# Performance work log

Hardware: AMD Instinct MI355X
Metric: run time of the kernel (lower is better)

## Reference

```python
import jax, jax.numpy as jnp
import numpy as np
from jax import lax

# Model dims (match init_kwargs / input_specs)
B, S, D = 4, 2048, 1024
L, H, K = 4, 4, 4
DH = D // H            # 256 head dim
UP = 1344              # ceil(1.3*D/64)*64, gated FFN proj dim
EPS = 1e-5


def _ln(x, w):
    # xlstm LayerNorm: weight only, no bias
    mu = x.mean(-1, keepdims=True)
    var = x.var(-1, keepdims=True)
    return (x - mu) * lax.rsqrt(var + EPS) * w


def _slstm_layer(xn, cw, cb, wi, wf, wz, wo, rk, b, gnw):
    # xn: (B,S,D). Causal depthwise conv1d + swish feeds i/f gates; z/o from xn.
    Bc, Sc, Dc = xn.shape
    xc = lax.conv_general_dilated(
        xn.transpose(0, 2, 1), cw[:, None, :], (1,), [(K - 1, 0)],
        dimension_numbers=("NCH", "OIH", "NCH"), feature_group_count=Dc)
    xc = jax.nn.silu(xc + cb[None, :, None]).transpose(0, 2, 1)
    hx = xc.reshape(Bc, Sc, H, DH)
    hz = xn.reshape(Bc, Sc, H, DH)
    # LinearHeadwiseExpand: block-diagonal per-head linear, no bias
    gi = jnp.einsum("bshd,hod->bsho", hx, wi)
    gf = jnp.einsum("bshd,hod->bsho", hx, wf)
    gz = jnp.einsum("bshd,hod->bsho", hz, wz)
    go = jnp.einsum("bshd,hod->bsho", hz, wo)
    wx = jnp.stack([gi, gf, gz, go], axis=3)  # (B,S,H,4,DH)

    def step(carry, wx_t):
        h, c, n, m = carry  # each (B,H,DH)
        raw = wx_t + jnp.einsum("bhd,hdgo->bhgo", h, rk) + b  # (B,H,4,DH)
        ir, fr, zr, og = raw[:, :, 0], raw[:, :, 1], raw[:, :, 2], raw[:, :, 3]
        lfm = m + jax.nn.log_sigmoid(fr)
        mn = jnp.maximum(ir, lfm)          # stabilizer state
        ig = jnp.exp(ir - mn)
        fg = jnp.exp(lfm - mn)
        cn = fg * c + ig * jnp.tanh(zr)
        nn = fg * n + ig
        hn = jax.nn.sigmoid(og) * cn / nn
        return (hn, cn, nn, mn), hn

    z0 = jnp.zeros((Bc, H, DH), xn.dtype)
    _, ys = lax.scan(step, (z0, z0, z0, z0), jnp.moveaxis(wx, 1, 0))
    y = jnp.moveaxis(ys, 0, 1)  # (B,S,H,DH)
    # MultiHeadLayerNorm / GroupNorm(num_groups=H), weight only
    mu = y.mean(-1, keepdims=True)
    var = y.var(-1, keepdims=True)
    y = (y - mu) * lax.rsqrt(var + EPS) * gnw.reshape(H, DH)
    return y.reshape(Bc, Sc, Dc)


def _ffn(xn, wu, wd):
    u = xn @ wu
    g, v = u[..., :UP], u[..., UP:]
    return (jax.nn.gelu(g, approximate=False) * v) @ wd


def setup_inputs() -> dict:
    key = jax.random.key(0)
    ks = jax.random.split(key, 9)
    sg = DH ** -0.5
    return {
        "x": jax.random.normal(ks[0], (B, S, D), jnp.float32),
        "ln1_w": jnp.ones((L, D), jnp.float32),
        "conv_w": jax.random.normal(ks[1], (L, D, K), jnp.float32) * 0.1,
        "conv_b": jnp.zeros((L, D), jnp.float32),
        "wi": jax.random.normal(ks[2], (L, H, DH, DH), jnp.float32) * sg,
        "wf": jax.random.normal(ks[3], (L, H, DH, DH), jnp.float32) * sg,
        "wz": jax.random.normal(ks[4], (L, H, DH, DH), jnp.float32) * sg,
        "wo": jax.random.normal(ks[5], (L, H, DH, DH), jnp.float32) * sg,
        "rker": jax.random.normal(ks[6], (L, H, DH, 4, DH), jnp.float32) * sg,
        "cell_b": jax.random.normal(ks[7], (L, H, 4, DH), jnp.float32) * 0.1,
        "gn_w": jnp.ones((L, D), jnp.float32),
        "ln2_w": jnp.ones((L, D), jnp.float32),
        "ff_up": jax.random.normal(ks[8], (L, D, 2 * UP), jnp.float32) * (D ** -0.5),
        "ff_down": jax.random.normal(jax.random.fold_in(key, 99), (L, UP, D), jnp.float32) * (UP ** -0.5),
        "post_w": jnp.ones((D,), jnp.float32),
    }


def reference(x, ln1_w, conv_w, conv_b, wi, wf, wz, wo, rker, cell_b, gn_w, ln2_w, ff_up, ff_down, post_w):
    for l in range(L):
        x = x + _slstm_layer(_ln(x, ln1_w[l]), conv_w[l], conv_b[l],
                             wi[l], wf[l], wz[l], wo[l], rker[l], cell_b[l], gn_w[l])
        x = x + _ffn(_ln(x, ln2_w[l]), ff_up[l], ff_down[l])
    return _ln(x, post_w)  # post-blocks norm; dropout is identity in eval
```

## Files before the change

### kernel.cpp

```cpp
#include <hip/hip_runtime.h>
#include <hip/hip_bf16.h>
#include <hip/hip_fp16.h>
#include <math.h>


typedef unsigned int  u32;
typedef unsigned short u16;
typedef __hip_bfloat16 bf16;

typedef short bf16x8 __attribute__((ext_vector_type(8)));
typedef float f32x4  __attribute__((ext_vector_type(4)));
typedef _Float16 half2t __attribute__((ext_vector_type(2)));

#define EPSF 1e-5f
#define SIGF32 0x3F800000u

__device__ __forceinline__ float bfu2f(u16 u){ return __uint_as_float(((u32)u) << 16); }
__device__ __forceinline__ float ldm(const void* p, long i, int f32){
  return f32 ? ((const float*)p)[i] : bfu2f(((const u16*)p)[i]);
}
__device__ __forceinline__ float qdot(u32 w, u32 hp, float acc){
#if defined(__has_builtin)
#if __has_builtin(__builtin_amdgcn_fdot2)
  return __builtin_amdgcn_fdot2(__builtin_bit_cast(half2t, w),
                                __builtin_bit_cast(half2t, hp), acc, false);
#else
  half2t a = __builtin_bit_cast(half2t, w);
  half2t b = __builtin_bit_cast(half2t, hp);
  acc = fmaf((float)a.x, (float)b.x, acc);
  return fmaf((float)a.y, (float)b.y, acc);
#endif
#else
  half2t a = __builtin_bit_cast(half2t, w);
  half2t b = __builtin_bit_cast(half2t, hp);
  acc = fmaf((float)a.x, (float)b.x, acc);
  return fmaf((float)a.y, (float)b.y, acc);
#endif
}

__global__ __launch_bounds__(256) void k_canary(const u32* __restrict__ sig,
                                                void* __restrict__ out, int n, float code){
  int f32 = (sig[0] == SIGF32);
  int i = blockIdx.x*256 + threadIdx.x;
  if (i >= n) return;
  float v = (i == 0) ? code : 0.f;
  if (f32) ((float*)out)[i] = v;
  else     ((bf16*)out)[i]  = __float2bfloat16(v);
}

__global__ __launch_bounds__(256) void k_cast(const void* __restrict__ in,
                                              const u32* __restrict__ sig,
                                              float* __restrict__ out){
  int f32 = (sig[0] == SIGF32);
  long i = (long)blockIdx.x*256 + threadIdx.x;
  if (f32){
    ((float4*)out)[i] = ((const float4*)in)[i];
  } else {
    ushort4 v = ((const ushort4*)in)[i];
    float4 f;
    f.x = bfu2f(v.x); f.y = bfu2f(v.y); f.z = bfu2f(v.z); f.w = bfu2f(v.w);
    ((float4*)out)[i] = f;
  }
}

__global__ __launch_bounds__(256) void k_cvt(const void* __restrict__ src, long off,
                                             const u32* __restrict__ sig,
                                             bf16* __restrict__ dst, int n){
  int f32 = (sig[0] == SIGF32);
  int i = blockIdx.x*256 + threadIdx.x;
  if (i < n) dst[i] = __float2bfloat16(ldm(src, off + i, f32));
}

__global__ __launch_bounds__(256) void k_ln(const float* __restrict__ X,
                                            const void* __restrict__ w, long woff,
                                            const u32* __restrict__ sig,
                                            void* __restrict__ out, int outf){
  int f32 = (sig[0] == SIGF32);
  int row = blockIdx.x, t = threadIdx.x;
  float4 xv = ((const float4*)(X + (long)row*1024))[t];
  float s1 = xv.x + xv.y + xv.z + xv.w;
  float s2 = xv.x*xv.x + xv.y*xv.y + xv.z*xv.z + xv.w*xv.w;
  #pragma unroll
  for (int off = 32; off >= 1; off >>= 1){ s1 += __shfl_xor(s1, off); s2 += __shfl_xor(s2, off); }
  __shared__ float rb[8];
  if ((t & 63) == 0){ rb[t>>6] = s1; rb[4 + (t>>6)] = s2; }
  __syncthreads();
  s1 = rb[0]+rb[1]+rb[2]+rb[3];
  s2 = rb[4]+rb[5]+rb[6]+rb[7];
  float mu  = s1 * (1.f/1024.f);
  float var = s2 * (1.f/1024.f) - mu*mu;
  float rs  = rsqrtf(fmaxf(var, 0.f) + EPSF);
  float xs[4] = {xv.x, xv.y, xv.z, xv.w};
  #pragma unroll
  for (int j = 0; j < 4; j++){
    float val = (xs[j]-mu)*rs*ldm(w, woff + t*4 + j, f32);
    long oi = (long)row*1024 + t*4 + j;
    if (outf && f32) ((float*)out)[oi] = val;
    else             ((bf16*)out)[oi]  = __float2bfloat16(val);
  }
}

__global__ __launch_bounds__(256) void k_conv(const bf16* __restrict__ XN,
                                              const void* __restrict__ cw, long cwoff,
                                              const void* __restrict__ cb, long cboff,
                                              const u32* __restrict__ sig,
                                              bf16* __restrict__ WX){
  int f32 = (sig[0] == SIGF32);
  int idx = blockIdx.x*256 + threadIdx.x;
  int c = idx & 1023;
  int s = (idx >> 10) & 2047;
  int b = idx >> 21;
  float acc = ldm(cb, cboff + c, f32);
  const bf16* xp = XN + idx;
  #pragma unroll
  for (int k = 0; k < 4; k++){
    int sk = s - 3 + k;
    float xv = (sk >= 0) ? (float)xp[(k-3)*1024] : 0.f;
    acc += xv * ldm(cw, cwoff + c*4 + k, f32);
  }
  float sg = 1.f / (1.f + __expf(-acc));
  WX[(long)b*8388608 + (long)(c>>8)*2097152 + (long)s*1024 + 512 + (c & 255)]
      = __float2bfloat16(acc * sg);
}

__global__ __launch_bounds__(256) void k_packrk(const void* __restrict__ rk, long off,
                                                const u32* __restrict__ sig,
                                                u32* __restrict__ rkReg,
                                                u32* __restrict__ rkLds,
                                                u32* __restrict__ rkStr){
  int f32 = (sig[0] == SIGF32);
  int idx = blockIdx.x*256 + threadIdx.x;
  if (idx >= 524288) return;
  int dp = idx & 127;
  int gc = (idx >> 7) & 1023;
  int h  = idx >> 17;
  long p = off + (long)h*262144 + (long)(dp*2)*1024 + gc;
  float a = ldm(rk, p, f32);
  float b = ldm(rk, p + 1024, f32);
  u32 lo = (u32)__builtin_bit_cast(u16, (_Float16)a);
  u32 hi = (u32)__builtin_bit_cast(u16, (_Float16)b);
  u32 v = lo | (hi << 16);
  if (dp < 64){
    rkReg[((long)dp*4 + h)*1024 + gc] = v;
  } else if (dp < 88){
    int k = (dp-64)>>2, j = (dp-64)&3;
    rkLds[((long)(h*6 + k)*1024 + gc)*4 + j] = v;
  } else {
    int pg = (dp-88)>>2, j = (dp-88)&3;
    rkStr[((long)(h*10 + pg)*1024 + gc)*4 + j] = v;
  }
}

__global__ __launch_bounds__(256) void k_transpose(const void* __restrict__ in, long off,
                                                   const u32* __restrict__ sig,
                                                   bf16* __restrict__ out, int R, int C){
  int f32 = (sig[0] == SIGF32);
  __shared__ bf16 tile[32][33];
  int tx = threadIdx.x & 31, ty = threadIdx.x >> 5;
  int r0 = blockIdx.y*32, c0 = blockIdx.x*32;
  #pragma unroll
  for (int i = 0; i < 4; i++)
    tile[ty + i*8][tx] = __float2bfloat16(ldm(in, off + (long)(r0 + ty + i*8)*C + c0 + tx, f32));
  __syncthreads();
  #pragma unroll
  for (int i = 0; i < 4; i++) out[(long)(c0 + ty + i*8)*R + r0 + tx] = tile[tx][ty + i*8];
}

__global__ __launch_bounds__(256) void k_gemm(const bf16* __restrict__ A, int lda, int aoff, int agate,
                                              const bf16* __restrict__ B0,
                                              const bf16* __restrict__ B1, int ldb, int nsplit,
                                              int K, int mode,
                                              bf16* __restrict__ outb, int ldo, int woff,
                                              float* __restrict__ resid){
  int lane = threadIdx.x & 63, wv = threadIdx.x >> 6;
  int wrow = wv >> 1, wcol = wv & 1;
  int m15 = lane & 15, q = lane >> 4;
  int mBase = blockIdx.x*128 + wrow*64;
  int nBase = blockIdx.y*128 + wcol*64;

  const bf16* Ap[4]; const bf16* Bp[4];
  #pragma unroll
  for (int i = 0; i < 4; i++){
    int row = mBase + i*16 + m15;
    long abase = agate ? ((long)(row >> 11)*8388608 + (long)(row & 2047)*1024)
                       : ((long)row*lda);
    Ap[i] = A + abase + aoff + q*8;
    int n = nBase + i*16 + m15;
    const bf16* bb = (n < nsplit) ? (B0 + (long)n*ldb) : (B1 + (long)(n - nsplit)*ldb);
    Bp[i] = bb + q*8;
  }
  f32x4 acc[4][4];
  f32x4 zero = {0.f, 0.f, 0.f, 0.f};
  #pragma unroll
  for (int i = 0; i < 4; i++)
    #pragma unroll
    for (int j = 0; j < 4; j++) acc[i][j] = zero;

  for (int k0 = 0; k0 < K; k0 += 32){
    bf16x8 af[4], bfg[4];
    #pragma unroll
    for (int i = 0; i < 4; i++){ af[i]  = *reinterpret_cast<const bf16x8*>(Ap[i]); Ap[i] += 32; }
    #pragma unroll
    for (int i = 0; i < 4; i++){ bfg[i] = *reinterpret_cast<const bf16x8*>(Bp[i]); Bp[i] += 32; }
    #pragma unroll
    for (int i = 0; i < 4; i++)
      #pragma unroll
      for (int j = 0; j < 4; j++)
        acc[i][j] = __builtin_amdgcn_mfma_f32_16x16x32_bf16(af[i], bfg[j], acc[i][j], 0, 0, 0);
  }

  #pragma unroll
  for (int i = 0; i < 4; i++){
    #pragma unroll
    for (int j = 0; j < 4; j++){
      #pragma unroll
      for (int r = 0; r < 4; r++){
        int row = mBase + i*16 + q*4 + r;
        int col = nBase + j*16 + m15;
        float v = acc[i][j][r];
        if (mode == 0){
          outb[(long)row*ldo + col] = __float2bfloat16(v);
        } else if (mode == 1){
          outb[(long)(row >> 11)*8388608 + (long)(row & 2047)*1024 + woff + col] = __float2bfloat16(v);
        } else {
          resid[(long)row*1024 + col] += v;
        }
      }
    }
  }
}

__global__ __launch_bounds__(256) void k_act(const bf16* __restrict__ U, bf16* __restrict__ E){
  int idx = blockIdx.x*256 + threadIdx.x;
  int row = idx / 1344;
  int j   = idx - row*1344;
  float g = (float)U[(long)row*2688 + j];
  float v = (float)U[(long)row*2688 + 1344 + j];
  float ge = 0.5f * g * (1.f + erff(g * 0.70710678118654752f));
  E[idx] = __float2bfloat16(ge * v);
}

__global__ __launch_bounds__(1024, 4) void k_recur(const bf16* __restrict__ WX,
                                                const u32*  __restrict__ rkReg,
                                                const uint4* __restrict__ rkLdsG,
                                                const uint4* __restrict__ rkStrG,
                                                const void* __restrict__ cb, long cboff,
                                                const void* __restrict__ gnw, long gnoff,
                                                const u32*  __restrict__ sig,
                                                float* __restrict__ X,
                                                int szero){
  int f32 = (sig[0] == SIGF32);
  int bh = blockIdx.x;
  int b = bh >> 2, h = bh & 3;
  int tid = threadIdx.x;
  int cell = tid & 255;

  u32 wreg[64];
  {
    const u32* rg = rkReg + h*1024 + tid;
    #pragma unroll
    for (int i = 0; i < 64; i++) wreg[i] = rg[i*4096];
  }
  #pragma unroll
  for (int i = 0; i < 64; i++) asm volatile("" : "+v"(wreg[i]));

  __shared__ __align__(16) uint4 wlds[6144];
  __shared__ __align__(16) float araw[1024];
  __shared__ __align__(16) u16 hs16[256];
  __shared__ float rbuf[8];
  {
    const uint4* srcL = rkLdsG + h*6144;
    #pragma unroll
    for (int k = 0; k < 6; k++) wlds[k*1024 + tid] = srcL[k*1024 + tid];
  }

  const uint4* st = rkStrG + h*10240 + tid;

  float bias = ldm(cb, cboff + h*1024 + tid, f32);
  float gw   = ldm(gnw, gnoff + h*256 + cell, f32);

  if (tid < 256) hs16[tid] = 0;
  __syncthreads();

  float c = 0.f, n = 0.f, m = 0.f;
  const u16* wxu = (const u16*)(WX + (long)bh*2097152) + tid;
  float* Xp = X + (long)b*2097152 + h*256 + cell;

  u16 wxc = wxu[0];
  for (int s = 0; s < 2048; s++){
    u16 wxn = wxu[(s < 2047) ? 1024 : 0];
    int off = s * szero;
    const uint4* hq = (const uint4*)hs16;

    float acc = bias + bfu2f(wxc);
    #pragma unroll
    for (int j2 = 0; j2 < 16; j2++){
      uint4 hv = hq[j2];
      acc = qdot(wreg[4*j2+0], hv.x, acc);
      acc = qdot(wreg[4*j2+1], hv.y, acc);
      acc = qdot(wreg[4*j2+2], hv.z, acc);
      acc = qdot(wreg[4*j2+3], hv.w, acc);
    }
    #pragma unroll
    for (int k = 0; k < 6; k++){
      uint4 q = wlds[k*1024 + tid + off];
      uint4 hv = hq[16+k];
      acc = qdot(q.x, hv.x, acc); acc = qdot(q.y, hv.y, acc);
      acc = qdot(q.z, hv.z, acc); acc = qdot(q.w, hv.w, acc);
    }
    #pragma unroll
    for (int pg = 0; pg < 10; pg++){
      uint4 q = st[pg*1024 + off];
      uint4 hv = hq[22+pg];
      acc = qdot(q.x, hv.x, acc); acc = qdot(q.y, hv.y, acc);
      acc = qdot(q.z, hv.z, acc); acc = qdot(q.w, hv.w, acc);
    }
    araw[tid] = acc;
    __syncthreads();

    float y = 0.f;
    if (tid < 256){
      float a0 = araw[cell], a1 = araw[256+cell], a2 = araw[512+cell], a3 = araw[768+cell];
      float e1   = __expf(-fabsf(a1));
      float lsig = fminf(a1, 0.f) - __logf(1.f + e1);
      float lfm  = m + lsig;
      float mn   = fmaxf(a0, lfm);
      float ig   = __expf(a0 - mn);
      float fg   = __expf(lfm - mn);
      float t2   = __expf(-2.f*fabsf(a2));
      float th   = __builtin_copysignf(__fdividef(1.f - t2, 1.f + t2), a2);
      float cn   = fg*c + ig*th;
      float nn   = fg*n + ig;
      float sg   = __fdividef(1.f, 1.f + __expf(-a3));
      float hn   = sg * __fdividef(cn, nn);
      c = cn; n = nn; m = mn;
      hs16[cell] = __builtin_bit_cast(u16, (_Float16)hn);
      float r1 = hn, r2 = hn*hn;
      #pragma unroll
      for (int o2 = 32; o2 >= 1; o2 >>= 1){ r1 += __shfl_xor(r1, o2); r2 += __shfl_xor(r2, o2); }
      if ((tid & 63) == 0){ rbuf[tid>>6] = r1; rbuf[4 + (tid>>6)] = r2; }
      y = hn;
    }
    __syncthreads();

    if (tid < 256){
      float S1 = rbuf[0]+rbuf[1]+rbuf[2]+rbuf[3];
      float S2 = rbuf[4]+rbuf[5]+rbuf[6]+rbuf[7];
      float mu  = S1 * (1.f/256.f);
      float var = S2 * (1.f/256.f) - mu*mu;
      *Xp += (y - mu) * rsqrtf(fmaxf(var, 0.f) + EPSF) * gw;
    }
    Xp += 1024;
    wxu += 1024;
    wxc = wxn;
  }
}

extern "C" void kernel_launch(void* const* d_in, const int* in_sizes, int n_in,
                              void* d_out, int out_size, void* d_ws, size_t ws_size,
                              hipStream_t stream){
  const void* x_in   = d_in[0];
  const void* ln1_w  = d_in[1];
  const void* conv_w = d_in[2];
  const void* conv_b = d_in[3];
  const void* wi     = d_in[4];
  const void* wf     = d_in[5];
  const void* wz     = d_in[6];
  const void* wo     = d_in[7];
  const void* rker   = d_in[8];
  const void* cell_b = d_in[9];
  const void* gn_w   = d_in[10];
  const void* ln2_w  = d_in[11];
  const void* ff_up  = d_in[12];
  const void* ff_dn  = d_in[13];
  const void* post_w = d_in[14];
  const u32* sig = (const u32*)ln1_w;

  if (ws_size < 134217728ULL){
    k_canary<<<(out_size+255)/256, 256, 0, stream>>>(sig, d_out, out_size, 4000.f);
    return;
  }
  if (n_in < 15 || in_sizes[0] != 8388608 || in_sizes[8] != 4194304 ||
      in_sizes[12] != 11010048 || out_size != 8388608){
    k_canary<<<(out_size+255)/256, 256, 0, stream>>>(sig, d_out, out_size, 8000.f);
    return;
  }

  char* ws = (char*)d_ws;
  float* X    = (float*)(ws + 0);
  bf16*  XN   = (bf16*) (ws + 33554432);
  u32*   rkReg= (u32*)  (ws + 50331648);
  u32*   rkLds= (u32*)  (ws + 50331648 + 1048576);
  u32*   rkStr= (u32*)  (ws + 50331648 + 1441792);
  bf16*  gW   = (bf16*) (ws + 50331648 + 2097152);
  bf16*  fupT = (bf16*) (ws + 50331648 + 4194304);
  bf16*  fdnT = (bf16*) (ws + 50331648 + 9699328);
  bf16*  WX   = (bf16*) (ws + 67108864);
  bf16*  U    = WX;
  bf16*  E    = (bf16*) (ws + 67108864 + 44040192);

  k_cast<<<8192, 256, 0, stream>>>(x_in, sig, X);

  for (int l = 0; l < 4; l++){
    k_ln<<<8192, 256, 0, stream>>>(X, ln1_w, (long)l*1024, sig, XN, 0);
    k_conv<<<32768, 256, 0, stream>>>(XN, conv_w, (long)l*4096, conv_b, (long)l*1024, sig, WX);

    k_cvt<<<1024, 256, 0, stream>>>(wi, (long)l*262144, sig, gW +      0, 262144);
    k_cvt<<<1024, 256, 0, stream>>>(wf, (long)l*262144, sig, gW + 262144, 262144);
    k_cvt<<<1024, 256, 0, stream>>>(wz, (long)l*262144, sig, gW + 524288, 262144);
    k_cvt<<<1024, 256, 0, stream>>>(wo, (long)l*262144, sig, gW + 786432, 262144);

    for (int h = 0; h < 4; h++){
      k_gemm<<<dim3(64,4), 256, 0, stream>>>(WX, 0, h*2097152 + 512, 1,
          gW + h*65536, gW + 262144 + h*65536, 256, 256,
          256, 1, WX, 0, h*2097152 + 0, nullptr);
    }
    k_packrk<<<2048, 256, 0, stream>>>(rker, (long)l*1048576, sig, rkReg, rkLds, rkStr);
    for (int h = 0; h < 4; h++){
      k_gemm<<<dim3(64,4), 256, 0, stream>>>(XN, 1024, h*256, 0,
          gW + 524288 + h*65536, gW + 786432 + h*65536, 256, 256,
          256, 1, WX, 0, h*2097152 + 512, nullptr);
    }

    k_recur<<<16, 1024, 0, stream>>>(WX, rkReg, (const uint4*)rkLds, (const uint4*)rkStr,
                                     cell_b, (long)l*4096, gn_w, (long)l*1024, sig, X, 0);

    k_ln<<<8192, 256, 0, stream>>>(X, ln2_w, (long)l*1024, sig, XN, 0);
    k_transpose<<<dim3(84,32), 256, 0, stream>>>(ff_up, (long)l*2752512, sig, fupT, 1024, 2688);
    k_gemm<<<dim3(64,21), 256, 0, stream>>>(XN, 1024, 0, 0, fupT, fupT, 1024, 1<<30,
        1024, 0, U, 2688, 0, nullptr);
    k_act<<<43008, 256, 0, stream>>>(U, E);
    k_transpose<<<dim3(32,42), 256, 0, stream>>>(ff_dn, (long)l*1376256, sig, fdnT, 1344, 1024);
    k_gemm<<<dim3(64,8), 256, 0, stream>>>(E, 1344, 0, 0, fdnT, fdnT, 1344, 1<<30,
        1344, 2, nullptr, 0, 0, X);
  }

  k_ln<<<8192, 256, 0, stream>>>(X, post_w, 0, sig, d_out, 1);
}
```

Measured before the change: 26.62 ms.

## Split recurrent matvec across four thread quarters and move GroupNorm to separate kernel

The recurrent kernel now assigns each thread a quarter of the hidden dimension for all four gates of a cell. Partial sums are reduced with cross-lane shuffles instead of being staged through shared memory. Register weights drop from 64 to 48 words per thread, and h is replicated into four padded shared copies to avoid bank conflicts. The per-step GroupNorm and residual add are taken out of the serial loop: hidden states are written as fp16 into the WX buffer and a new parallel k_gn kernel applies the norm afterwards. In exchange each step does more shuffles and strided global loads, and the norm adds an extra kernel with its own memory traffic.

```diff
diff --git a/kernel.cpp b/kernel.cpp
--- a/kernel.cpp
+++ b/kernel.cpp
@@ -19,6 +19,7 @@
 __device__ __forceinline__ float ldm(const void* p, long i, int f32){
   return f32 ? ((const float*)p)[i] : bfu2f(((const u16*)p)[i]);
 }
+__device__ __forceinline__ float f16u2f(u16 u){ return (float)__builtin_bit_cast(_Float16, u); }
 __device__ __forceinline__ float qdot(u32 w, u32 hp, float acc){
 #if defined(__has_builtin)
 #if __has_builtin(__builtin_amdgcn_fdot2)
@@ -134,20 +135,22 @@
   int dp = idx & 127;
   int gc = (idx >> 7) & 1023;
   int h  = idx >> 17;
+  int g  = gc >> 8, cell = gc & 255;
+  int q  = dp >> 5, i = dp & 31;
+  int tid = (cell >> 4)*64 + q*16 + (cell & 15);
   long p = off + (long)h*262144 + (long)(dp*2)*1024 + gc;
   float a = ldm(rk, p, f32);
   float b = ldm(rk, p + 1024, f32);
   u32 lo = (u32)__builtin_bit_cast(u16, (_Float16)a);
   u32 hi = (u32)__builtin_bit_cast(u16, (_Float16)b);
   u32 v = lo | (hi << 16);
-  if (dp < 64){
-    rkReg[((long)dp*4 + h)*1024 + gc] = v;
-  } else if (dp < 88){
-    int k = (dp-64)>>2, j = (dp-64)&3;
-    rkLds[((long)(h*6 + k)*1024 + gc)*4 + j] = v;
+  if (i < 12){
+    rkReg[((long)(g*12 + i)*4 + h)*1024 + tid] = v;
+  } else if (i < 16){
+    rkLds[(((long)(h*4 + g))*1024 + tid)*4 + (i - 12)] = v;
   } else {
-    int pg = (dp-88)>>2, j = (dp-88)&3;
-    rkStr[((long)(h*10 + pg)*1024 + gc)*4 + j] = v;
+    int c = (i-16) >> 2, j = (i-16) & 3;
+    rkStr[(((long)(h*16 + g*4 + c))*1024 + tid)*4 + j] = v;
   }
 }
 
@@ -240,87 +243,98 @@
   E[idx] = __float2bfloat16(ge * v);
 }
 
-__global__ __launch_bounds__(1024, 4) void k_recur(const bf16* __restrict__ WX,
+__global__ __launch_bounds__(1024, 4) void k_recur(bf16* __restrict__ WX,
                                                 const u32*  __restrict__ rkReg,
                                                 const uint4* __restrict__ rkLdsG,
                                                 const uint4* __restrict__ rkStrG,
                                                 const void* __restrict__ cb, long cboff,
-                                                const void* __restrict__ gnw, long gnoff,
                                                 const u32*  __restrict__ sig,
-                                                float* __restrict__ X,
                                                 int szero){
   int f32 = (sig[0] == SIGF32);
   int bh = blockIdx.x;
-  int b = bh >> 2, h = bh & 3;
+  int h = bh & 3;
   int tid = threadIdx.x;
-  int cell = tid & 255;
-
-  u32 wreg[64];
+  int celllo = tid & 15, q = (tid >> 4) & 3, cellhi = tid >> 6;
+  int cell = cellhi*16 + celllo;
+
+  u32 wreg[48];
   {
     const u32* rg = rkReg + h*1024 + tid;
     #pragma unroll
-    for (int i = 0; i < 64; i++) wreg[i] = rg[i*4096];
-  }
-  #pragma unroll
-  for (int i = 0; i < 64; i++) asm volatile("" : "+v"(wreg[i]));
-
-  __shared__ __align__(16) uint4 wlds[6144];
-  __shared__ __align__(16) float araw[1024];
-  __shared__ __align__(16) u16 hs16[256];
-  __shared__ float rbuf[8];
+    for (int i = 0; i < 48; i++) wreg[i] = rg[i*4096];
+  }
+  #pragma unroll
+  for (int i = 0; i < 48; i++) asm volatile("" : "+v"(wreg[i]));
+
+  __shared__ __align__(16) uint4 wlds[4096];
+  __shared__ __align__(16) u16 hsr[4*264];
   {
-    const uint4* srcL = rkLdsG + h*6144;
-    #pragma unroll
-    for (int k = 0; k < 6; k++) wlds[k*1024 + tid] = srcL[k*1024 + tid];
-  }
-
-  const uint4* st = rkStrG + h*10240 + tid;
-
-  float bias = ldm(cb, cboff + h*1024 + tid, f32);
-  float gw   = ldm(gnw, gnoff + h*256 + cell, f32);
-
-  if (tid < 256) hs16[tid] = 0;
+    const uint4* srcL = rkLdsG + h*4096;
+    #pragma unroll
+    for (int g = 0; g < 4; g++) wlds[g*1024 + tid] = srcL[g*1024 + tid];
+  }
+  if (tid < 528) ((u32*)hsr)[tid] = 0;
+
+  const uint4* st = rkStrG + h*16384 + tid;
+  float bias = ldm(cb, cboff + h*1024 + q*256 + cell, f32);
+
   __syncthreads();
 
   float c = 0.f, n = 0.f, m = 0.f;
-  const u16* wxu = (const u16*)(WX + (long)bh*2097152) + tid;
-  float* Xp = X + (long)b*2097152 + h*256 + cell;
+  const u16* wxu = (const u16*)WX + (long)bh*2097152 + q*256 + cell;
+  u16* yout = (u16*)WX + (long)bh*2097152 + cell;
 
   u16 wxc = wxu[0];
   for (int s = 0; s < 2048; s++){
     u16 wxn = wxu[(s < 2047) ? 1024 : 0];
     int off = s * szero;
-    const uint4* hq = (const uint4*)hs16;
-
-    float acc = bias + bfu2f(wxc);
-    #pragma unroll
-    for (int j2 = 0; j2 < 16; j2++){
-      uint4 hv = hq[j2];
-      acc = qdot(wreg[4*j2+0], hv.x, acc);
-      acc = qdot(wreg[4*j2+1], hv.y, acc);
-      acc = qdot(wreg[4*j2+2], hv.z, acc);
-      acc = qdot(wreg[4*j2+3], hv.w, acc);
+
+    const uint4* hq = ((const uint4*)hsr) + q*41;
+    uint4 hh0 = hq[0+off], hh1 = hq[1+off], hh2 = hq[2+off], hh3 = hq[3+off];
+    uint4 hh4 = hq[4+off], hh5 = hq[5+off], hh6 = hq[6+off], hh7 = hq[7+off];
+
+    float p0, p1, p2, p3;
+    #pragma unroll
+    for (int g = 0; g < 4; g++){
+      uint4 s0 = st[(g*4+0)*1024 + off];
+      uint4 s1 = st[(g*4+1)*1024 + off];
+      uint4 s2 = st[(g*4+2)*1024 + off];
+      uint4 s3 = st[(g*4+3)*1024 + off];
+      uint4 wl = wlds[g*1024 + tid + off];
+      const u32* wr = wreg + g*12;
+      float a = 0.f;
+      a = qdot(wr[0],  hh0.x, a); a = qdot(wr[1],  hh0.y, a);
+      a = qdot(wr[2],  hh0.z, a); a = qdot(wr[3],  hh0.w, a);
+      a = qdot(wr[4],  hh1.x, a); a = qdot(wr[5],  hh1.y, a);
+      a = qdot(wr[6],  hh1.z, a); a = qdot(wr[7],  hh1.w, a);
+      a = qdot(wr[8],  hh2.x, a); a = qdot(wr[9],  hh2.y, a);
+      a = qdot(wr[10], hh2.z, a); a = qdot(wr[11], hh2.w, a);
+      a = qdot(wl.x, hh3.x, a); a = qdot(wl.y, hh3.y, a);
+      a = qdot(wl.z, hh3.z, a); a = qdot(wl.w, hh3.w, a);
+      a = qdot(s0.x, hh4.x, a); a = qdot(s0.y, hh4.y, a);
+      a = qdot(s0.z, hh4.z, a); a = qdot(s0.w, hh4.w, a);
+      a = qdot(s1.x, hh5.x, a); a = qdot(s1.y, hh5.y, a);
+      a = qdot(s1.z, hh5.z, a); a = qdot(s1.w, hh5.w, a);
+      a = qdot(s2.x, hh6.x, a); a = qdot(s2.y, hh6.y, a);
+      a = qdot(s2.z, hh6.z, a); a = qdot(s2.w, hh6.w, a);
+      a = qdot(s3.x, hh7.x, a); a = qdot(s3.y, hh7.y, a);
+      a = qdot(s3.z, hh7.z, a); a = qdot(s3.w, hh7.w, a);
+      if (g == 0) p0 = a; else if (g == 1) p1 = a; else if (g == 2) p2 = a; else p3 = a;
     }
-    #pragma unroll
-    for (int k = 0; k < 6; k++){
-      uint4 q = wlds[k*1024 + tid + off];
-      uint4 hv = hq[16+k];
-      acc = qdot(q.x, hv.x, acc); acc = qdot(q.y, hv.y, acc);
-      acc = qdot(q.z, hv.z, acc); acc = qdot(q.w, hv.w, acc);
-    }
-    #pragma unroll
-    for (int pg = 0; pg < 10; pg++){
-      uint4 q = st[pg*1024 + off];
-      uint4 hv = hq[22+pg];
-      acc = qdot(q.x, hv.x, acc); acc = qdot(q.y, hv.y, acc);
-      acc = qdot(q.z, hv.z, acc); acc = qdot(q.w, hv.w, acc);
-    }
-    araw[tid] = acc;
+    float addv = bias + bfu2f(wxc);
+    p0 += (q == 0) ? addv : 0.f;
+    p1 += (q == 1) ? addv : 0.f;
+    p2 += (q == 2) ? addv : 0.f;
+    p3 += (q == 3) ? addv : 0.f;
+    p0 += __shfl_xor(p0, 16); p0 += __shfl_xor(p0, 32);
+    p1 += __shfl_xor(p1, 16); p1 += __shfl_xor(p1, 32);
+    p2 += __shfl_xor(p2, 16); p2 += __shfl_xor(p2, 32);
+    p3 += __shfl_xor(p3, 16); p3 += __shfl_xor(p3, 32);
+
     __syncthreads();
 
-    float y = 0.f;
-    if (tid < 256){
-      float a0 = araw[cell], a1 = araw[256+cell], a2 = araw[512+cell], a3 = araw[768+cell];
+    if (q == 0){
+      float a0 = p0, a1 = p1, a2 = p2, a3 = p3;
       float e1   = __expf(-fabsf(a1));
       float lsig = fminf(a1, 0.f) - __logf(1.f + e1);
       float lfm  = m + lsig;
@@ -334,26 +348,40 @@
       float sg   = __fdividef(1.f, 1.f + __expf(-a3));
       float hn   = sg * __fdividef(cn, nn);
       c = cn; n = nn; m = mn;
-      hs16[cell] = __builtin_bit_cast(u16, (_Float16)hn);
-      float r1 = hn, r2 = hn*hn;
-      #pragma unroll
-      for (int o2 = 32; o2 >= 1; o2 >>= 1){ r1 += __shfl_xor(r1, o2); r2 += __shfl_xor(r2, o2); }
-      if ((tid & 63) == 0){ rbuf[tid>>6] = r1; rbuf[4 + (tid>>6)] = r2; }
-      y = hn;
+      u16 h16 = __builtin_bit_cast(u16, (_Float16)hn);
+      hsr[0*264 + cell] = h16; hsr[1*264 + cell] = h16;
+      hsr[2*264 + cell] = h16; hsr[3*264 + cell] = h16;
+      yout[(long)s*1024] = h16;
     }
     __syncthreads();
 
-    if (tid < 256){
-      float S1 = rbuf[0]+rbuf[1]+rbuf[2]+rbuf[3];
-      float S2 = rbuf[4]+rbuf[5]+rbuf[6]+rbuf[7];
-      float mu  = S1 * (1.f/256.f);
-      float var = S2 * (1.f/256.f) - mu*mu;
-      *Xp += (y - mu) * rsqrtf(fmaxf(var, 0.f) + EPSF) * gw;
-    }
-    Xp += 1024;
     wxu += 1024;
     wxc = wxn;
   }
+}
+
+__global__ __launch_bounds__(256) void k_gn(const u16* __restrict__ Y,
+                                            const void* __restrict__ gnw, long gnoff,
+                                            const u32* __restrict__ sig,
+                                            float* __restrict__ X){
+  int f32 = (sig[0] == SIGF32);
+  int r = blockIdx.x;
+  int bh = r >> 11, s = r & 2047, b = bh >> 2, h = bh & 3;
+  int t = threadIdx.x;
+  float y = f16u2f(Y[(long)bh*2097152 + (long)s*1024 + t]);
+  float s1 = y, s2 = y*y;
+  #pragma unroll
+  for (int off = 32; off >= 1; off >>= 1){ s1 += __shfl_xor(s1, off); s2 += __shfl_xor(s2, off); }
+  __shared__ float rb[8];
+  if ((t & 63) == 0){ rb[t>>6] = s1; rb[4 + (t>>6)] = s2; }
+  __syncthreads();
+  s1 = rb[0]+rb[1]+rb[2]+rb[3];
+  s2 = rb[4]+rb[5]+rb[6]+rb[7];
+  float mu  = s1 * (1.f/256.f);
+  float var = s2 * (1.f/256.f) - mu*mu;
+  float rs  = rsqrtf(fmaxf(var, 0.f) + EPSF);
+  float gw  = ldm(gnw, gnoff + h*256 + t, f32);
+  X[(long)b*2097152 + (long)s*1024 + h*256 + t] += (y - mu)*rs*gw;
 }
 
 extern "C" void kernel_launch(void* const* d_in, const int* in_sizes, int n_in,
@@ -390,8 +418,8 @@
   float* X    = (float*)(ws + 0);
   bf16*  XN   = (bf16*) (ws + 33554432);
   u32*   rkReg= (u32*)  (ws + 50331648);
-  u32*   rkLds= (u32*)  (ws + 50331648 + 1048576);
-  u32*   rkStr= (u32*)  (ws + 50331648 + 1441792);
+  u32*   rkLds= (u32*)  (ws + 50331648 + 786432);
+  u32*   rkStr= (u32*)  (ws + 50331648 + 1048576);
   bf16*  gW   = (bf16*) (ws + 50331648 + 2097152);
   bf16*  fupT = (bf16*) (ws + 50331648 + 4194304);
   bf16*  fdnT = (bf16*) (ws + 50331648 + 9699328);
@@ -423,7 +451,8 @@
     }
 
     k_recur<<<16, 1024, 0, stream>>>(WX, rkReg, (const uint4*)rkLds, (const uint4*)rkStr,
-                                     cell_b, (long)l*4096, gn_w, (long)l*1024, sig, X, 0);
+                                     cell_b, (long)l*4096, sig, 0);
+    k_gn<<<32768, 256, 0, stream>>>((const u16*)WX, gn_w, (long)l*1024, sig, X);
 
     k_ln<<<8192, 256, 0, stream>>>(X, ln2_w, (long)l*1024, sig, XN, 0);
     k_transpose<<<dim3(84,32), 256, 0, stream>>>(ff_up, (long)l*2752512, sig, fupT, 1024, 2688);
```

Result: slower. 28.74 ms (+8.0%).
